# Kernel tuning notes

Hardware: AMD Instinct MI355X
Metric: run time of the kernel (lower is better)

The kernel has to match this reference:

```python
import jax, jax.numpy as jnp
import numpy as np

N = 100000
E = 1600000
D_IN = 128
D_OUT = 128


def setup_inputs() -> dict:
    key = jax.random.key(0)
    k1, k2, k3, k4 = jax.random.split(key, 4)
    x = jax.random.normal(k1, (N, D_IN), dtype=jnp.float32)
    edge_index = jax.random.randint(k2, (2, E), 0, N, dtype=jnp.int64)
    # GCNConv params: glorot weight, zero bias
    scale = jnp.sqrt(6.0 / (D_IN + D_OUT)).astype(jnp.float32)
    W = jax.random.uniform(k3, (D_IN, D_OUT), dtype=jnp.float32, minval=-scale, maxval=scale)
    b = jnp.zeros((D_OUT,), dtype=jnp.float32)
    return {"x": x, "edge_index": edge_index, "W": W, "b": b}


def reference(x, edge_index, W, b):
    n = x.shape[0]
    # add self-loops (PyG GCNConv default: add_self_loops=True)
    loops = jnp.arange(n, dtype=edge_index.dtype)
    src = jnp.concatenate([edge_index[0], loops])
    dst = jnp.concatenate([edge_index[1], loops])
    # symmetric normalization: deg computed at target nodes
    ones = jnp.ones_like(dst, dtype=x.dtype)
    deg = jax.ops.segment_sum(ones, dst, num_segments=n)
    dinv = jnp.where(deg > 0, jax.lax.rsqrt(deg), 0.0)
    norm = dinv[src] * dinv[dst]  # [E+N]
    # linear transform then gather-scale-scatter aggregation
    h = x @ W  # [N, D_OUT]
    msgs = h[src] * norm[:, None]  # [E+N, D_OUT]
    out = jax.ops.segment_sum(msgs, dst, num_segments=n)
    return out + b
```

## Files before the change

### kernel.cpp

```cpp
#include <hip/hip_runtime.h>

#define D 128
#define CAP 5120

typedef __attribute__((ext_vector_type(4))) float f32x4;
typedef __attribute__((ext_vector_type(8))) short s16x8;

static __device__ __forceinline__ ushort f2bf(float f) {
    unsigned u = __float_as_uint(f);
    u += 0x7fffu + ((u >> 16) & 1u);
    return (ushort)(u >> 16);
}
static __device__ __forceinline__ float bf2f(ushort s) {
    return __uint_as_float(((unsigned)s) << 16);
}

__global__ __launch_bounds__(1024) void k_part(const int* __restrict__ src,
                                               const int* __restrict__ dst,
                                               int e, int nbins,
                                               int* __restrict__ gcursor,
                                               unsigned* __restrict__ praw) {
    __shared__ int hist[512];
    int tid = threadIdx.x;
    for (int j = tid; j < nbins; j += 1024) hist[j] = 0;
    __syncthreads();

    int chunk = (e + gridDim.x - 1) / gridDim.x;
    int lo = blockIdx.x * chunk;
    int hi = lo + chunk; if (hi > e) hi = e;

    for (int i = lo + tid; i < hi; i += 1024)
        atomicAdd(&hist[dst[i] >> 8], 1);
    __syncthreads();

    for (int j = tid; j < nbins; j += 1024)
        hist[j] = atomicAdd(&gcursor[j], hist[j]);
    __syncthreads();

    for (int i = lo + tid; i < hi; i += 1024) {
        int d = dst[i];
        int bin = d >> 8;
        int pos = atomicAdd(&hist[bin], 1);
        if (pos < CAP)
            praw[(size_t)bin * CAP + pos] = ((unsigned)(d & 255) << 24) | (unsigned)src[i];
    }
}

__global__ __launch_bounds__(1024) void k_fine(unsigned* __restrict__ praw,
                                               const int* __restrict__ gcursor,
                                               int n,
                                               int* __restrict__ deg,
                                               float* __restrict__ dinv,
                                               int* __restrict__ offs) {
    __shared__ int hist[256], scanv[256], cur[256];
    __shared__ unsigned stage[CAP];
    int b = blockIdx.x, tid = threadIdx.x;
    int base = b * CAP;
    int cnt = gcursor[b]; if (cnt > CAP) cnt = CAP;

    if (tid < 256) hist[tid] = 0;
    __syncthreads();
    for (int i = tid; i < cnt; i += 1024)
        atomicAdd(&hist[praw[base + i] >> 24], 1);
    __syncthreads();

    if (tid < 256) scanv[tid] = hist[tid];
    __syncthreads();
    for (int off = 1; off < 256; off <<= 1) {
        int t = 0;
        if (tid < 256 && tid >= off) t = scanv[tid - off];
        __syncthreads();
        if (tid < 256) scanv[tid] += t;
        __syncthreads();
    }
    if (tid < 256) {
        int ex = scanv[tid] - hist[tid];
        cur[tid] = ex;
        int d0 = b * 256 + tid;
        if (d0 < n) {
            deg[d0]  = hist[tid];
            dinv[d0] = rsqrtf((float)hist[tid] + 1.f);
            offs[d0] = base + ex;
        }
    }
    __syncthreads();

    for (int i = tid; i < cnt; i += 1024) {
        unsigned p = praw[base + i];
        int pos = atomicAdd(&cur[p >> 24], 1);
        stage[pos] = p & 0xFFFFFFu;
    }
    __syncthreads();
    for (int i = tid; i < cnt; i += 1024)
        praw[base + i] = stage[i];
}

__global__ __launch_bounds__(256) void k_wt(const float* __restrict__ W,
                                            ushort* __restrict__ WT) {
    int i = blockIdx.x * 256 + threadIdx.x;
    int nn = i >> 7, k = i & 127;
    WT[i] = f2bf(W[k * D + nn]);
}

__global__ __launch_bounds__(256, 2) void k_gemm_mfma(const float* __restrict__ x,
                                                      const ushort* __restrict__ WT,
                                                      const float* __restrict__ dinv,
                                                      ushort* __restrict__ h,
                                                      int n, int nchunks) {
    int lane = threadIdx.x & 63;
    int wid  = threadIdx.x >> 6;
    int lr = lane & 15;
    int lk = lane >> 4;

    s16x8 bfrag[8][4];
#pragma unroll
    for (int nt = 0; nt < 8; ++nt)
#pragma unroll
        for (int kk = 0; kk < 4; ++kk)
            bfrag[nt][kk] = *reinterpret_cast<const s16x8*>(
                WT + (nt * 16 + lr) * D + kk * 32 + lk * 8);

    int stride = gridDim.x * 4;
    for (int chunk = blockIdx.x * 4 + wid; chunk < nchunks; chunk += stride) {
        int r0 = chunk * 16;
        int ar = r0 + lr;
        if (ar > n - 1) ar = n - 1;

        s16x8 afrag[4];
#pragma unroll
        for (int kk = 0; kk < 4; ++kk) {
            const float4* p = reinterpret_cast<const float4*>(x) +
                              (size_t)ar * 32 + kk * 8 + lk * 2;
            float4 u = p[0];
            float4 v = p[1];
            s16x8 a;
            a[0] = (short)f2bf(u.x); a[1] = (short)f2bf(u.y);
            a[2] = (short)f2bf(u.z); a[3] = (short)f2bf(u.w);
            a[4] = (short)f2bf(v.x); a[5] = (short)f2bf(v.y);
            a[6] = (short)f2bf(v.z); a[7] = (short)f2bf(v.w);
            afrag[kk] = a;
        }

        f32x4 acc[8];
#pragma unroll
        for (int nt = 0; nt < 8; ++nt) acc[nt] = (f32x4){0.f, 0.f, 0.f, 0.f};

#pragma unroll
        for (int kk = 0; kk < 4; ++kk)
#pragma unroll
            for (int nt = 0; nt < 8; ++nt)
                acc[nt] = __builtin_amdgcn_mfma_f32_16x16x32_bf16(
                    afrag[kk], bfrag[nt][kk], acc[nt], 0, 0, 0);

#pragma unroll
        for (int i = 0; i < 4; ++i) {
            int row = r0 + lk * 4 + i;
            if (row < n) {
                float di = dinv[row];
#pragma unroll
                for (int nt = 0; nt < 8; ++nt)
                    h[(size_t)row * D + nt * 16 + lr] = f2bf(acc[nt][i] * di);
            }
        }
    }
}

__global__ __launch_bounds__(256) void k_gather(const unsigned* __restrict__ pairs,
                                                const int* __restrict__ offs,
                                                const int* __restrict__ deg,
                                                const float* __restrict__ dinv,
                                                const ushort* __restrict__ h,
                                                const float* __restrict__ b,
                                                float* __restrict__ out, int n) {
    int g = (blockIdx.x * 256 + threadIdx.x) >> 5;
    if (g >= n) return;
    int lane = threadIdx.x & 31;
    const ushort4* h4 = reinterpret_cast<const ushort4*>(h);

    ushort4 hv = h4[(size_t)g * 32 + lane];
    float ax = bf2f(hv.x), ay = bf2f(hv.y), az = bf2f(hv.z), aw = bf2f(hv.w);

    int start = offs[g];
    int cnt   = deg[g];
    int k = 0;
    for (; k + 1 < cnt; k += 2) {
        int s0 = (int)pairs[start + k];
        int s1 = (int)pairs[start + k + 1];
        ushort4 v0 = h4[(size_t)s0 * 32 + lane];
        ushort4 v1 = h4[(size_t)s1 * 32 + lane];
        ax += bf2f(v0.x) + bf2f(v1.x);
        ay += bf2f(v0.y) + bf2f(v1.y);
        az += bf2f(v0.z) + bf2f(v1.z);
        aw += bf2f(v0.w) + bf2f(v1.w);
    }
    if (k < cnt) {
        int s0 = (int)pairs[start + k];
        ushort4 v0 = h4[(size_t)s0 * 32 + lane];
        ax += bf2f(v0.x); ay += bf2f(v0.y); az += bf2f(v0.z); aw += bf2f(v0.w);
    }

    float dd = dinv[g];
    float4 bv = reinterpret_cast<const float4*>(b)[lane];
    float4 o;
    o.x = ax * dd + bv.x;
    o.y = ay * dd + bv.y;
    o.z = az * dd + bv.z;
    o.w = aw * dd + bv.w;
    reinterpret_cast<float4*>(out)[(size_t)g * 32 + lane] = o;
}

extern "C" void kernel_launch(void* const* d_in, const int* in_sizes, int n_in,
                              void* d_out, int out_size, void* d_ws, size_t ws_size,
                              hipStream_t stream) {
    const float* x  = (const float*)d_in[0];
    const int*   ei = (const int*)d_in[1];
    const float* W  = (const float*)d_in[2];
    const float* b  = (const float*)d_in[3];
    float* out = (float*)d_out;

    int n = in_sizes[0] / D;
    int e = in_sizes[1] / 2;
    const int* src = ei;
    const int* dst = ei + e;
    int nbins = (n + 255) >> 8;

    char* ws = (char*)d_ws;
    ushort*   h       = (ushort*)ws;    ws += (size_t)n * D * 2;
    ushort*   WT      = (ushort*)ws;    ws += (size_t)D * D * 2;
    int*      deg     = (int*)ws;       ws += (size_t)n * 4;
    float*    dinv    = (float*)ws;     ws += (size_t)n * 4;
    int*      offs    = (int*)ws;       ws += (size_t)n * 4;
    int*      gcursor = (int*)ws;       ws += 512 * 4;
    unsigned* praw    = (unsigned*)ws;

    hipMemsetAsync(gcursor, 0, 512 * 4, stream);

    k_part<<<256, 1024, 0, stream>>>(src, dst, e, nbins, gcursor, praw);

    k_fine<<<nbins, 1024, 0, stream>>>(praw, gcursor, n, deg, dinv, offs);

    k_wt<<<64, 256, 0, stream>>>(W, WT);

    int nchunks = (n + 15) / 16;
    k_gemm_mfma<<<512, 256, 0, stream>>>(x, WT, dinv, h, n, nchunks);

    int nb = (n * 32 + 255) / 256;
    k_gather<<<nb, 256, 0, stream>>>(praw, offs, deg, dinv, h, b, out, n);
}
```

Before: 129.3 us.

## Slice h into 16-column panels and gather per panel for cache locality

The GEMM now writes h in a column-sliced layout, 8 panels of 16 bf16 columns, each contiguous over nodes. The gather kernel assigns each block one panel and processes 4 nodes per 8-lane group, so each random neighbor read touches a 32-byte segment of a 3.2MB panel. The aim is to keep the working set of concurrently running blocks in L2/LLC and cut cache misses on the irregular gather. In exchange, each edge's index list is read 8 times, and each read is only 32 bytes wide, which may underuse memory transactions.

```diff
diff --git a/kernel.cpp b/kernel.cpp
--- a/kernel.cpp
+++ b/kernel.cpp
@@ -2,6 +2,7 @@
 
 #define D 128
 #define CAP 5120
+#define NPG 4
 
 typedef __attribute__((ext_vector_type(4))) float f32x4;
 typedef __attribute__((ext_vector_type(8))) short s16x8;
@@ -159,7 +160,8 @@
                 float di = dinv[row];
 #pragma unroll
                 for (int nt = 0; nt < 8; ++nt)
-                    h[(size_t)row * D + nt * 16 + lr] = f2bf(acc[nt][i] * di);
+                    h[(size_t)nt * n * 16 + (size_t)row * 16 + lr] =
+                        f2bf(acc[nt][i] * di);
             }
         }
     }
@@ -172,41 +174,47 @@
                                                 const ushort* __restrict__ h,
                                                 const float* __restrict__ b,
                                                 float* __restrict__ out, int n) {
-    int g = (blockIdx.x * 256 + threadIdx.x) >> 5;
-    if (g >= n) return;
-    int lane = threadIdx.x & 31;
-    const ushort4* h4 = reinterpret_cast<const ushort4*>(h);
-
-    ushort4 hv = h4[(size_t)g * 32 + lane];
-    float ax = bf2f(hv.x), ay = bf2f(hv.y), az = bf2f(hv.z), aw = bf2f(hv.w);
-
-    int start = offs[g];
-    int cnt   = deg[g];
-    int k = 0;
-    for (; k + 1 < cnt; k += 2) {
-        int s0 = (int)pairs[start + k];
-        int s1 = (int)pairs[start + k + 1];
-        ushort4 v0 = h4[(size_t)s0 * 32 + lane];
-        ushort4 v1 = h4[(size_t)s1 * 32 + lane];
-        ax += bf2f(v0.x) + bf2f(v1.x);
-        ay += bf2f(v0.y) + bf2f(v1.y);
-        az += bf2f(v0.z) + bf2f(v1.z);
-        aw += bf2f(v0.w) + bf2f(v1.w);
-    }
-    if (k < cnt) {
-        int s0 = (int)pairs[start + k];
-        ushort4 v0 = h4[(size_t)s0 * 32 + lane];
-        ax += bf2f(v0.x); ay += bf2f(v0.y); az += bf2f(v0.z); aw += bf2f(v0.w);
-    }
-
-    float dd = dinv[g];
-    float4 bv = reinterpret_cast<const float4*>(b)[lane];
-    float4 o;
-    o.x = ax * dd + bv.x;
-    o.y = ay * dd + bv.y;
-    o.z = az * dd + bv.z;
-    o.w = aw * dd + bv.w;
-    reinterpret_cast<float4*>(out)[(size_t)g * 32 + lane] = o;
+    int s    = blockIdx.x & 7;
+    int blk  = blockIdx.x >> 3;
+    int grp  = threadIdx.x >> 3;
+    int lane = threadIdx.x & 7;
+
+    const ushort* hs = h + (size_t)s * n * 16 + lane * 2;
+    float2 bv = *reinterpret_cast<const float2*>(b + s * 16 + lane * 2);
+
+    int node = (blk * 32 + grp) * NPG;
+#pragma unroll 1
+    for (int j = 0; j < NPG; ++j, ++node) {
+        if (node >= n) return;
+        int st  = offs[node];
+        int cnt = deg[node];
+
+        unsigned v = *reinterpret_cast<const unsigned*>(hs + (size_t)node * 16);
+        float a0 = bf2f((ushort)v);
+        float a1 = bf2f((ushort)(v >> 16));
+
+        int k = 0;
+        for (; k + 1 < cnt; k += 2) {
+            int s0 = (int)pairs[st + k];
+            int s1 = (int)pairs[st + k + 1];
+            unsigned v0 = *reinterpret_cast<const unsigned*>(hs + (size_t)s0 * 16);
+            unsigned v1 = *reinterpret_cast<const unsigned*>(hs + (size_t)s1 * 16);
+            a0 += bf2f((ushort)v0) + bf2f((ushort)v1);
+            a1 += bf2f((ushort)(v0 >> 16)) + bf2f((ushort)(v1 >> 16));
+        }
+        if (k < cnt) {
+            int s0 = (int)pairs[st + k];
+            unsigned v0 = *reinterpret_cast<const unsigned*>(hs + (size_t)s0 * 16);
+            a0 += bf2f((ushort)v0);
+            a1 += bf2f((ushort)(v0 >> 16));
+        }
+
+        float dd = dinv[node];
+        float2 o;
+        o.x = a0 * dd + bv.x;
+        o.y = a1 * dd + bv.y;
+        *reinterpret_cast<float2*>(out + (size_t)node * D + s * 16 + lane * 2) = o;
+    }
 }
 
 extern "C" void kernel_launch(void* const* d_in, const int* in_sizes, int n_in,
@@ -244,6 +252,7 @@
     int nchunks = (n + 15) / 16;
     k_gemm_mfma<<<512, 256, 0, stream>>>(x, WT, dinv, h, n, nchunks);
 
-    int nb = (n * 32 + 255) / 256;
+    int nodes_per_blk = 32 * NPG;
+    int nb = 8 * ((n + nodes_per_blk - 1) / nodes_per_blk);
     k_gather<<<nb, 256, 0, stream>>>(praw, offs, deg, dinv, h, b, out, n);
 }
```

After: 201.5 us. 55.8% more time.
